# Kernel optimization log

Hardware: AMD Instinct MI355X
Metric: run time of the kernel (lower is better)

## Reference

```python
import jax, jax.numpy as jnp
import numpy as np

B, C, H = 256, 5, 13
N_AGENTS = 8192
N_EDGES = 262144
ACT = 21


def setup_inputs() -> dict:
    key = jax.random.key(0)
    ks = jax.random.split(key, 20)
    inp = {
        "x": jax.random.normal(ks[0], (B, C, H, H), jnp.float32),
        "x_msg": jax.random.normal(ks[1], (N_AGENTS,), jnp.float32),
        "edge_index": jax.random.randint(ks[2], (N_EDGES, 2), 0, N_AGENTS, jnp.int64 if jax.config.jax_enable_x64 else jnp.int32),
        "action": jax.random.randint(ks[3], (B,), 0, ACT, jnp.int32),
        # params (orthogonal init approximated by scaled normal; math identical)
        "conv1_w": jax.random.normal(ks[4], (32, 5, 3, 3), jnp.float32) * 0.1,
        "conv1_b": jnp.zeros((32,), jnp.float32),
        "conv2_w": jax.random.normal(ks[5], (64, 32, 3, 3), jnp.float32) * 0.05,
        "conv2_b": jnp.zeros((64,), jnp.float32),
        "fc_w": jax.random.normal(ks[6], (512, 1024), jnp.float32) * 0.03,
        "fc_b": jnp.zeros((512,), jnp.float32),
        "fc_mu_w": jax.random.normal(ks[7], (ACT, 512), jnp.float32) * 0.01,
        "fc_mu_b": jnp.zeros((ACT,), jnp.float32),
        "msg_w": jax.random.normal(ks[8], (N_AGENTS, 512), jnp.float32) * 0.01,
        "msg_b": jnp.zeros((N_AGENTS,), jnp.float32),
        "gcn1_w": jax.random.normal(ks[9], (2, 16), jnp.float32) * 0.5,
        "gcn1_b": jnp.zeros((16,), jnp.float32),
        "gcn2_w": jax.random.normal(ks[10], (16, N_AGENTS), jnp.float32) * 0.1,
        "gcn2_b": jnp.zeros((N_AGENTS,), jnp.float32),
    }
    return inp


def _gcn_norm(edge_index, n):
    # add self-loops; edge_index is (E,2) [src, dst]
    loops = jnp.arange(n, dtype=edge_index.dtype)
    src = jnp.concatenate([edge_index[:, 0], loops])
    dst = jnp.concatenate([edge_index[:, 1], loops])
    deg = jax.ops.segment_sum(jnp.ones_like(src, jnp.float32), dst, num_segments=n)
    dinv = jnp.where(deg > 0, jax.lax.rsqrt(deg), 0.0)
    norm = dinv[src] * dinv[dst]  # [E+n]
    return src, dst, norm


def _gcn_conv(h, src, dst, norm, W, b, n):
    hw = h @ W  # [n, out]
    out = jax.ops.segment_sum(norm[:, None] * hw[src], dst, num_segments=n)
    return out + b


def reference(x, x_msg, edge_index, action, conv1_w, conv1_b, conv2_w, conv2_b,
              fc_w, fc_b, fc_mu_w, fc_mu_b, msg_w, msg_b,
              gcn1_w, gcn1_b, gcn2_w, gcn2_b):
    dn = ("NCHW", "OIHW", "NCHW")
    h = jax.lax.conv_general_dilated(x, conv1_w, (2, 2), "VALID", dimension_numbers=dn)
    h = jax.nn.relu(h + conv1_b[None, :, None, None])  # [B,32,6,6]
    h = jax.lax.conv_general_dilated(h, conv2_w, (1, 1), "VALID", dimension_numbers=dn)
    h = jax.nn.relu(h + conv2_b[None, :, None, None])  # [B,64,4,4]
    h = h.reshape(h.shape[0], -1)  # [B,1024], torch NCHW flatten order
    hidden = jax.nn.relu(h @ fc_w.T + fc_b)  # [B,512]

    logits = hidden @ fc_mu_w.T + fc_mu_b            # [B,21]
    actor_encoding = hidden @ msg_w.T + msg_b        # [B,N]

    # Categorical log_prob / entropy for the given action
    logp = jax.nn.log_softmax(logits, axis=-1)
    log_prob = jnp.take_along_axis(logp, action[:, None], axis=1)[:, 0]
    entropy = -jnp.sum(jnp.exp(logp) * logp, axis=-1)

    # GNN message branch (eval mode: dropout is identity)
    feats = jnp.stack([x_msg, actor_encoding[0]], axis=0).T  # [N,2]
    n = feats.shape[0]
    src, dst, norm = _gcn_norm(edge_index, n)
    g = jax.nn.relu(_gcn_conv(feats, src, dst, norm, gcn1_w, gcn1_b, n))  # [N,16]
    g = _gcn_conv(g, src, dst, norm, gcn2_w, gcn2_b, n)                    # [N,N]
    msg_out = jax.nn.log_softmax(g, axis=1).mean(axis=1)                   # [N]

    return (action, msg_out, log_prob, entropy)
```

## Files before the change

kernel.cpp:

```cpp
#include <hip/hip_runtime.h>
#include <hip/hip_bf16.h>

#define NB 256
#define NACT 21
#define NA 8192
#define NE 262144
#define CSR_CAP 128
#define LOG2E 1.44269504f

#if __has_builtin(__builtin_amdgcn_exp2f)
#define EXP2F(x) __builtin_amdgcn_exp2f(x)
#else
#define EXP2F(x) exp2f(x)
#endif

typedef __attribute__((ext_vector_type(8))) short short8;
typedef __attribute__((ext_vector_type(4))) float float4v;

__device__ inline float wsum64(float v) {
#pragma unroll
  for (int m = 32; m > 0; m >>= 1) v += __shfl_xor(v, m, 64);
  return v;
}

__device__ inline unsigned short f2bf(float f) {
  union { __hip_bfloat16 h; unsigned short u; } cv;
  cv.h = __float2bfloat16(f);
  return cv.u;
}

__global__ __launch_bounds__(512, 2) void k_ip(
    const float* __restrict__ x, const float* __restrict__ c1w, const float* __restrict__ c1b_,
    const float* __restrict__ c2w, const float* __restrict__ fcw,
    const float* __restrict__ g2w, const float* __restrict__ g2b,
    unsigned short* c1b, unsigned short* w2abf, int* cnt,
    unsigned short* fcwbf, unsigned short* w2t, float* wpart) {
  __shared__ float sm[3437];
  int t = threadIdx.x, b = blockIdx.x;
  if (b >= 308) {
    float (*red)[17] = (float(*)[17])sm;
    float* b2s = sm + 272;
    int blk = b - 308;
    {
      int base = (blk * 512 + t) * 2;
      float2 v = *(const float2*)&fcw[base];
      fcwbf[base + 0] = f2bf(v.x);
      fcwbf[base + 1] = f2bf(v.y);
    }
    {
      if (t < 256) {
        int jj = t >> 4, k = t & 15;
        int j = blk * 16 + jj;
        float w = g2w[k * 8192 + j];
        w2t[j * 16 + k] = f2bf(w);
        red[jj][k] = w;
      }
      if (t < 16) b2s[t] = g2b[blk * 16 + t];
      __syncthreads();
      if (t < 16) {
        float s = 0.0f;
#pragma unroll
        for (int q = 0; q < 16; q++) s += red[q][t];
        wpart[blk * 17 + t] = s;
      } else if (t == 16) {
        float s = 0.0f;
#pragma unroll
        for (int q = 0; q < 16; q++) s += b2s[q];
        wpart[blk * 17 + 16] = s;
      }
    }
    return;
  }
  if (b >= 272) {
    int i = (b - 272) * 512 + t;
    w2abf[i] = f2bf(c2w[i]);
    return;
  }
  if (b >= 256) {
    cnt[(b - 256) * 512 + t] = 0;
    return;
  }
  float* xs = sm;
  float* w1s = sm + 845;
  float* c1s = sm + 2285;
  for (int i = t; i < 845; i += 512) xs[i] = x[b * 845 + i];
  for (int i = t; i < 1440; i += 512) w1s[i] = c1w[i];
  __syncthreads();
  for (int idx = t; idx < 1152; idx += 512) {
    int oc = idx / 36, p = idx - oc * 36;
    int oy = p / 6, ox = p - oy * 6;
    float acc = c1b_[oc];
    const float* wp = &w1s[oc * 45];
#pragma unroll
    for (int ic = 0; ic < 5; ic++)
#pragma unroll
      for (int ky = 0; ky < 3; ky++)
#pragma unroll
        for (int kx = 0; kx < 3; kx++)
          acc += xs[ic * 169 + (oy * 2 + ky) * 13 + ox * 2 + kx] * wp[ic * 9 + ky * 3 + kx];
    c1s[idx] = fmaxf(acc, 0.0f);
  }
  __syncthreads();
  for (int i = t; i < 4608; i += 512) {
    int p = i / 288, k = i - p * 288;
    int ic = k / 9, r = k - ic * 9;
    int ky = r / 3, kx = r - ky * 3;
    int oy = p >> 2, ox = p & 3;
    c1b[b * 4608 + i] = f2bf(c1s[ic * 36 + (oy + ky) * 6 + ox + kx]);
  }
}

__global__ __launch_bounds__(512, 2) void k_cf(
    const int* __restrict__ edges, int* cnt, int* csr,
    const unsigned short* __restrict__ c1b, const unsigned short* __restrict__ w2abf,
    const float* __restrict__ c2b, const unsigned short* __restrict__ fcwbf,
    const float* __restrict__ fcb, const float* __restrict__ wpart,
    float* hidden, float* wsf) {
  __shared__ __align__(16) unsigned short hs[16384];
  __shared__ __align__(16) unsigned short w2a[18432];
  __shared__ float red[2048];
  int t = threadIdx.x, blk = blockIdx.x;
  int wave = t >> 6, lane = t & 63;
  int m = lane & 15, quad = lane >> 4;
  if (blk >= 1024) {
    if (t < 272) {
      int q = t / 17, c = t - q * 17;
      float s = 0.0f;
      for (int r = q; r < 512; r += 16) s += wpart[r * 17 + c];
      red[t] = s;
    }
    __syncthreads();
    if (t < 17) {
      float s = 0.0f;
#pragma unroll
      for (int q = 0; q < 16; q++) s += red[q * 17 + t];
      wsf[t] = s;
    }
    return;
  }
  if (blk >= 512) {
    int e = (blk - 512) * 512 + t;
    int s = edges[2 * e], d = edges[2 * e + 1];
    int slot = atomicAdd(&cnt[d], 1);
    if (slot < CSR_CAP) csr[d * CSR_CAP + slot] = s;
    return;
  }
  for (int i = t; i < 2304; i += 512)
    *(short8*)&w2a[i * 8] = *(const short8*)&w2abf[i * 8];
  __syncthreads();
  int tr = blk >> 5, tc = blk & 31;
  {
    int nlb = wave * 32;
    int nbase = tr * 256 + nlb;
    float4v z = {0.0f, 0.0f, 0.0f, 0.0f};
    float4v acc00 = z, acc01 = z, acc02 = z, acc03 = z;
    float4v acc10 = z, acc11 = z, acc12 = z, acc13 = z;
#pragma unroll
    for (int ks = 0; ks < 9; ks++) {
      int ko = ks * 32 + quad * 8;
      short8 a0 = *(const short8*)&w2a[(0 * 16 + m) * 288 + ko];
      short8 a1 = *(const short8*)&w2a[(1 * 16 + m) * 288 + ko];
      short8 a2 = *(const short8*)&w2a[(2 * 16 + m) * 288 + ko];
      short8 a3 = *(const short8*)&w2a[(3 * 16 + m) * 288 + ko];
      short8 b0 = *(const short8*)&c1b[(nbase + m) * 288 + ko];
      short8 b1 = *(const short8*)&c1b[(nbase + 16 + m) * 288 + ko];
      acc00 = __builtin_amdgcn_mfma_f32_16x16x32_bf16(a0, b0, acc00, 0, 0, 0);
      acc01 = __builtin_amdgcn_mfma_f32_16x16x32_bf16(a1, b0, acc01, 0, 0, 0);
      acc02 = __builtin_amdgcn_mfma_f32_16x16x32_bf16(a2, b0, acc02, 0, 0, 0);
      acc03 = __builtin_amdgcn_mfma_f32_16x16x32_bf16(a3, b0, acc03, 0, 0, 0);
      acc10 = __builtin_amdgcn_mfma_f32_16x16x32_bf16(a0, b1, acc10, 0, 0, 0);
      acc11 = __builtin_amdgcn_mfma_f32_16x16x32_bf16(a1, b1, acc11, 0, 0, 0);
      acc12 = __builtin_amdgcn_mfma_f32_16x16x32_bf16(a2, b1, acc12, 0, 0, 0);
      acc13 = __builtin_amdgcn_mfma_f32_16x16x32_bf16(a3, b1, acc13, 0, 0, 0);
    }
    float4v accs[2][4] = {{acc00, acc01, acc02, acc03}, {acc10, acc11, acc12, acc13}};
#pragma unroll
    for (int nt = 0; nt < 2; nt++) {
#pragma unroll
      for (int mt = 0; mt < 4; mt++) {
#pragma unroll
        for (int r = 0; r < 4; r++) {
          int oc = mt * 16 + quad * 4 + r;
          int nl = nlb + nt * 16 + m;
          hs[(nl >> 4) * 1024 + oc * 16 + (nl & 15)] =
              f2bf(fmaxf(accs[nt][mt][r] + c2b[oc], 0.0f));
        }
      }
    }
  }
  __syncthreads();
  {
    const unsigned short* ap = &hs[m * 1024 + wave * 128 + quad * 8];
    const unsigned short* bp = &fcwbf[(tc * 16 + m) * 1024 + wave * 128 + quad * 8];
    float4v acc = {0.0f, 0.0f, 0.0f, 0.0f};
#pragma unroll
    for (int ks = 0; ks < 4; ks++) {
      short8 av = *(const short8*)(ap + ks * 32);
      short8 bv = *(const short8*)(bp + ks * 32);
      acc = __builtin_amdgcn_mfma_f32_16x16x32_bf16(av, bv, acc, 0, 0, 0);
    }
#pragma unroll
    for (int r = 0; r < 4; r++) red[wave * 256 + (quad * 4 + r) * 16 + m] = acc[r];
    __syncthreads();
    if (t < 256) {
      float s = 0.0f;
#pragma unroll
      for (int w = 0; w < 8; w++) s += red[w * 256 + t];
      int gr = tr * 16 + (t >> 4);
      int gc = tc * 16 + (t & 15);
      hidden[gr * 512 + gc] = fmaxf(s + fcb[gc], 0.0f);
    }
  }
}

__global__ __launch_bounds__(512, 2) void k_he(
    const float* __restrict__ hidden, const float* __restrict__ muw,
    const float* __restrict__ mub, const float* __restrict__ msgw,
    const float* __restrict__ msgb, const int* __restrict__ cnt,
    const float* __restrict__ x_msg, const int* __restrict__ action,
    float2* xe, float* dinv, float* out) {
  __shared__ float muT[10752];
  __shared__ float hrows[2048];
  int t = threadIdx.x, blk = blockIdx.x;
  int wave = t >> 6, lane = t & 63;
  if (blk >= 512) {
    int i = (blk - 512) * 512 + t;
    float d = rsqrtf((float)cnt[i] + 1.0f);
    dinv[i] = d;
    xe[i].x = d * x_msg[i];
    return;
  }
  if (blk < 64) {
    int b0 = blk * 4;
    for (int i = t; i < 10752; i += 512) {
      int a = i >> 9, k = i & 511;
      muT[k * 21 + a] = muw[i];
    }
    for (int i = t; i < 2048; i += 512) hrows[i] = hidden[b0 * 512 + i];
    __syncthreads();
    if (wave < 4) {
      int b = b0 + wave;
      float logit = -1e30f;
      if (lane < NACT) {
        float acc = mub[lane];
        const float* hr = &hrows[wave * 512];
        for (int k = 0; k < 512; k++) acc += hr[k] * muT[k * 21 + lane];
        logit = acc;
      }
      float mx = logit;
#pragma unroll
      for (int s = 32; s > 0; s >>= 1) mx = fmaxf(mx, __shfl_xor(mx, s, 64));
      float e = (lane < NACT) ? __expf(logit - mx) : 0.0f;
      float se = wsum64(e);
      float swl = wsum64(e * logit);
      float lse = mx + __logf(se);
      int act = action[b];
      if (lane == 0) {
        out[b] = (float)act;
        out[8704 + b] = lse - swl / se;
      }
      if (lane == act) out[8448 + b] = logit - lse;
    }
  } else {
    int wg = (blk - 64) * 8 + wave;
    for (int j = wg; j < NA; j += 3584) {
      const float* wp = &msgw[j * 512 + lane * 8];
      float4 w0 = *(const float4*)(wp);
      float4 w1 = *(const float4*)(wp + 4);
      float4 h0 = *(const float4*)&hidden[lane * 8];
      float4 h1 = *(const float4*)&hidden[lane * 8 + 4];
      float s = w0.x * h0.x + w0.y * h0.y + w0.z * h0.z + w0.w * h0.w +
                w1.x * h1.x + w1.y * h1.y + w1.z * h1.z + w1.w * h1.w;
      s = wsum64(s);
      if (lane == 0) xe[j].y = rsqrtf((float)cnt[j] + 1.0f) * (s + msgb[j]);
    }
  }
}

__global__ __launch_bounds__(512, 4) void k_g1(
    const int* __restrict__ cnt, const int* __restrict__ csr,
    const float* __restrict__ dinv, const float2* __restrict__ xe,
    const float* __restrict__ g1w, const float* __restrict__ g1b, float* gbuf2) {
  int t = threadIdx.x, blk = blockIdx.x;
  int wave = t >> 6, lane = t & 63;
  int wg = blk * 8 + wave;
#pragma unroll
  for (int rr = 0; rr < 2; rr++) {
    int i = wg * 2 + rr;
    int ci = min(cnt[i], CSR_CAP);
    float di = dinv[i];
    float a0 = 0.0f, a1 = 0.0f;
    for (int e = lane; e < ci; e += 64) {
      int s = csr[i * CSR_CAP + e];
      float2 v = xe[s];
      a0 += v.x;
      a1 += v.y;
    }
    float2 vi = xe[i];
    float f0 = (wsum64(a0) + vi.x) * di;
    float f1 = (wsum64(a1) + vi.y) * di;
    if (lane < 16) {
      float gv = fmaxf(f0 * g1w[lane] + f1 * g1w[16 + lane] + g1b[lane], 0.0f);
      gbuf2[i * 16 + lane] = di * gv;
    }
  }
}

__global__ __launch_bounds__(512, 4) void k_msg(
    const int* __restrict__ cnt, const int* __restrict__ csr,
    const float* __restrict__ dinv, const float* __restrict__ gbuf2,
    const float* __restrict__ wsf, const unsigned short* __restrict__ w2t,
    const float* __restrict__ g2b, float* out) {
  __shared__ __align__(16) unsigned short vbf[256];
  __shared__ float vf[256];
  __shared__ float pl[2048];
  __shared__ float sl[128];
  __shared__ float wsfs[17];
  int t = threadIdx.x, blk = blockIdx.x;
  int wave = t >> 6, lane = t & 63;
  int rowbase = blk * 16;
  if (t < 17) wsfs[t] = wsf[t];
  {
    int eq = lane >> 4, c = lane & 15;
#pragma unroll
    for (int rr = 0; rr < 2; rr++) {
      int il = wave * 2 + rr;
      int i = rowbase + il;
      int ci = min(cnt[i], CSR_CAP);
      float di = dinv[i];
      float acc = (eq == 0) ? gbuf2[i * 16 + c] : 0.0f;
      for (int e = eq; e < ci; e += 4) {
        int s = csr[i * CSR_CAP + e];
        acc += gbuf2[s * 16 + c];
      }
      acc *= di;
      acc += __shfl_xor(acc, 16, 64);
      acc += __shfl_xor(acc, 32, 64);
      if (eq == 0) {
        vf[il * 16 + c] = acc;
        vbf[il * 16 + c] = f2bf(acc * LOG2E);
      }
    }
  }
  __syncthreads();
  float myMean = 0.0f;
  if (t < 16) {
    float dot = 0.0f;
#pragma unroll
    for (int c = 0; c < 16; c++) dot += vf[t * 16 + c] * wsfs[c];
    myMean = (dot + wsfs[16]) * (1.0f / 8192.0f);
  }
  {
    int quad = lane >> 4, n = lane & 15;
    int k8 = quad * 8;
    short8 za = {0, 0, 0, 0, 0, 0, 0, 0};
    short8 a1 = za;
    if (quad < 2) a1 = *(const short8*)&vbf[n * 16 + k8];
    float sacc[4];
#pragma unroll
    for (int q = 0; q < 4; q++) sacc[q] = 0.0f;
    int colb = wave * 1024 + n;
    for (int tp = 0; tp < 64; tp += 2) {
      int col1 = colb + tp * 16;
      int col2 = col1 + 16;
      short8 b1 = za, b2 = za;
      if (quad < 2) {
        b1 = *(const short8*)&w2t[col1 * 16 + k8];
        b2 = *(const short8*)&w2t[col2 * 16 + k8];
      }
      float bb1 = g2b[col1] * LOG2E, bb2 = g2b[col2] * LOG2E;
      float4v c1 = {bb1, bb1, bb1, bb1};
      float4v c2 = {bb2, bb2, bb2, bb2};
      float4v s11 = __builtin_amdgcn_mfma_f32_16x16x32_bf16(a1, b1, c1, 0, 0, 0);
      float4v s12 = __builtin_amdgcn_mfma_f32_16x16x32_bf16(a1, b2, c2, 0, 0, 0);
#pragma unroll
      for (int r = 0; r < 4; r++) sacc[r] += EXP2F(s11[r]) + EXP2F(s12[r]);
    }
#pragma unroll
    for (int q = 0; q < 4; q++) {
      int rl = quad * 4 + q;
      pl[rl * 128 + wave * 16 + n] = sacc[q];
    }
  }
  __syncthreads();
  if (t < 128) {
    int r = t >> 3, seg = t & 7;
    int base = r * 128 + seg * 16;
    float ll = 0.0f;
#pragma unroll
    for (int i = 0; i < 16; i++) ll += pl[base + i];
    sl[r * 8 + seg] = ll;
  }
  __syncthreads();
  if (t < 16) {
    float ll = 0.0f;
#pragma unroll
    for (int i = 0; i < 8; i++) ll += sl[t * 8 + i];
    out[256 + rowbase + t] = myMean - __logf(ll);
  }
}

extern "C" void kernel_launch(void* const* d_in, const int* in_sizes, int n_in,
                              void* d_out, int out_size, void* d_ws, size_t ws_size,
                              hipStream_t stream) {
  const float* x     = (const float*)d_in[0];
  const float* x_msg = (const float*)d_in[1];
  const int*   edges = (const int*)d_in[2];
  const int*   action= (const int*)d_in[3];
  const float* c1w   = (const float*)d_in[4];
  const float* c1bb  = (const float*)d_in[5];
  const float* c2w   = (const float*)d_in[6];
  const float* c2b   = (const float*)d_in[7];
  const float* fcw   = (const float*)d_in[8];
  const float* fcb   = (const float*)d_in[9];
  const float* muw   = (const float*)d_in[10];
  const float* mub   = (const float*)d_in[11];
  const float* msgw  = (const float*)d_in[12];
  const float* msgb  = (const float*)d_in[13];
  const float* g1w   = (const float*)d_in[14];
  const float* g1b   = (const float*)d_in[15];
  const float* g2w   = (const float*)d_in[16];
  const float* g2b   = (const float*)d_in[17];
  float* out = (float*)d_out;

  float* ws     = (float*)d_ws;
  unsigned short* fcwbf   = (unsigned short*)(ws + 131072);
  float* hidden = ws + 393216;
  float2* xe    = (float2*)(ws + 524288);
  float* dinv   = ws + 540672;
  float* gbuf2  = ws + 548864;
  float* wpart  = ws + 679936;
  unsigned short* w2t = (unsigned short*)(ws + 688640);
  int*   cnt    = (int*)(ws + 754176);
  int*   csr    = (int*)(ws + 762368);
  float* wsf    = ws + 1810944;
  unsigned short* c1b   = (unsigned short*)(ws + 1810964);
  unsigned short* w2abf = (unsigned short*)(ws + 2400788);

  k_ip <<<820, 512, 0, stream>>>(x, c1w, c1bb, c2w, fcw, g2w, g2b,
                                 c1b, w2abf, cnt, fcwbf, w2t, wpart);
  k_cf <<<1025, 512, 0, stream>>>(edges, cnt, csr, c1b, w2abf, c2b,
                                  fcwbf, fcb, wpart, hidden, wsf);
  k_he <<<528, 512, 0, stream>>>(hidden, muw, mub, msgw, msgb, cnt, x_msg,
                                 action, xe, dinv, out);
  k_g1 <<<512, 512, 0, stream>>>(cnt, csr, dinv, xe, g1w, g1b, gbuf2);
  k_msg<<<512, 512, 0, stream>>>(cnt, csr, dinv, gbuf2, wsf, w2t, g2b, out);
}
```

Baseline: 170.4 us.

## Fuse conv2 into per-sample conv1 kernel and drop redundant conv2 recompute

Moves the conv2 MFMA from k_cf into k_ip, where each sample block now computes conv2 directly from its shared-memory im2col tile, converting the fp32 conv2 weights to bf16 on the fly. Only the 1024-wide bf16 activations go to global memory, instead of the larger im2col buffer and a separate bf16 weight buffer. Before, every k_cf block (32 per row-tile) recomputed the same conv2 tile; now k_cf only runs the fc GEMM and uses less shared memory (launch bounds raised to 4). In exchange, k_ip blocks do more work, with only 4 of 8 waves active for conv2, and every block re-reads and re-converts the conv2 weights from global memory.

After: 165.2 us. 1.03x faster.

```diff
diff --git a/kernel.cpp b/kernel.cpp
--- a/kernel.cpp
+++ b/kernel.cpp
@@ -31,16 +31,17 @@
 
 __global__ __launch_bounds__(512, 2) void k_ip(
     const float* __restrict__ x, const float* __restrict__ c1w, const float* __restrict__ c1b_,
-    const float* __restrict__ c2w, const float* __restrict__ fcw,
+    const float* __restrict__ c2w, const float* __restrict__ c2b, const float* __restrict__ fcw,
     const float* __restrict__ g2w, const float* __restrict__ g2b,
-    unsigned short* c1b, unsigned short* w2abf, int* cnt,
+    unsigned short* h1024bf, int* cnt,
     unsigned short* fcwbf, unsigned short* w2t, float* wpart) {
-  __shared__ float sm[3437];
+  __shared__ __align__(16) float sm[5744];
   int t = threadIdx.x, b = blockIdx.x;
-  if (b >= 308) {
+  int wave = t >> 6, lane = t & 63;
+  if (b >= 272) {
     float (*red)[17] = (float(*)[17])sm;
     float* b2s = sm + 272;
-    int blk = b - 308;
+    int blk = b - 272;
     {
       int base = (blk * 512 + t) * 2;
       float2 v = *(const float2*)&fcw[base];
@@ -71,11 +72,6 @@
     }
     return;
   }
-  if (b >= 272) {
-    int i = (b - 272) * 512 + t;
-    w2abf[i] = f2bf(c2w[i]);
-    return;
-  }
   if (b >= 256) {
     cnt[(b - 256) * 512 + t] = 0;
     return;
@@ -83,6 +79,7 @@
   float* xs = sm;
   float* w1s = sm + 845;
   float* c1s = sm + 2285;
+  unsigned short* c1bf = (unsigned short*)(sm + 3440);
   for (int i = t; i < 845; i += 512) xs[i] = x[b * 845 + i];
   for (int i = t; i < 1440; i += 512) w1s[i] = c1w[i];
   __syncthreads();
@@ -103,21 +100,42 @@
   __syncthreads();
   for (int i = t; i < 4608; i += 512) {
     int p = i / 288, k = i - p * 288;
-    int ic = k / 9, r = k - ic * 9;
-    int ky = r / 3, kx = r - ky * 3;
+    int ic = k / 9, rr = k - ic * 9;
+    int ky = rr / 3, kx = rr - ky * 3;
     int oy = p >> 2, ox = p & 3;
-    c1b[b * 4608 + i] = f2bf(c1s[ic * 36 + (oy + ky) * 6 + ox + kx]);
-  }
-}
-
-__global__ __launch_bounds__(512, 2) void k_cf(
+    c1bf[i] = f2bf(c1s[ic * 36 + (oy + ky) * 6 + ox + kx]);
+  }
+  __syncthreads();
+  if (wave < 4) {
+    int m = lane & 15, quad = lane >> 4;
+    float4v acc = {0.0f, 0.0f, 0.0f, 0.0f};
+#pragma unroll
+    for (int ks = 0; ks < 9; ks++) {
+      int ko = ks * 32 + quad * 8;
+      const float* ar = &c2w[(wave * 16 + m) * 288 + ko];
+      float4 af0 = *(const float4*)ar;
+      float4 af1 = *(const float4*)(ar + 4);
+      short8 a;
+      a[0] = (short)f2bf(af0.x); a[1] = (short)f2bf(af0.y);
+      a[2] = (short)f2bf(af0.z); a[3] = (short)f2bf(af0.w);
+      a[4] = (short)f2bf(af1.x); a[5] = (short)f2bf(af1.y);
+      a[6] = (short)f2bf(af1.z); a[7] = (short)f2bf(af1.w);
+      short8 bv = *(const short8*)&c1bf[m * 288 + ko];
+      acc = __builtin_amdgcn_mfma_f32_16x16x32_bf16(a, bv, acc, 0, 0, 0);
+    }
+#pragma unroll
+    for (int r = 0; r < 4; r++) {
+      int oc = wave * 16 + quad * 4 + r;
+      h1024bf[b * 1024 + oc * 16 + m] = f2bf(fmaxf(acc[r] + c2b[oc], 0.0f));
+    }
+  }
+}
+
+__global__ __launch_bounds__(512, 4) void k_cf(
     const int* __restrict__ edges, int* cnt, int* csr,
-    const unsigned short* __restrict__ c1b, const unsigned short* __restrict__ w2abf,
-    const float* __restrict__ c2b, const unsigned short* __restrict__ fcwbf,
+    const unsigned short* __restrict__ h1024bf, const unsigned short* __restrict__ fcwbf,
     const float* __restrict__ fcb, const float* __restrict__ wpart,
     float* hidden, float* wsf) {
-  __shared__ __align__(16) unsigned short hs[16384];
-  __shared__ __align__(16) unsigned short w2a[18432];
   __shared__ float red[2048];
   int t = threadIdx.x, blk = blockIdx.x;
   int wave = t >> 6, lane = t & 63;
@@ -145,71 +163,26 @@
     if (slot < CSR_CAP) csr[d * CSR_CAP + slot] = s;
     return;
   }
-  for (int i = t; i < 2304; i += 512)
-    *(short8*)&w2a[i * 8] = *(const short8*)&w2abf[i * 8];
-  __syncthreads();
   int tr = blk >> 5, tc = blk & 31;
-  {
-    int nlb = wave * 32;
-    int nbase = tr * 256 + nlb;
-    float4v z = {0.0f, 0.0f, 0.0f, 0.0f};
-    float4v acc00 = z, acc01 = z, acc02 = z, acc03 = z;
-    float4v acc10 = z, acc11 = z, acc12 = z, acc13 = z;
-#pragma unroll
-    for (int ks = 0; ks < 9; ks++) {
-      int ko = ks * 32 + quad * 8;
-      short8 a0 = *(const short8*)&w2a[(0 * 16 + m) * 288 + ko];
-      short8 a1 = *(const short8*)&w2a[(1 * 16 + m) * 288 + ko];
-      short8 a2 = *(const short8*)&w2a[(2 * 16 + m) * 288 + ko];
-      short8 a3 = *(const short8*)&w2a[(3 * 16 + m) * 288 + ko];
-      short8 b0 = *(const short8*)&c1b[(nbase + m) * 288 + ko];
-      short8 b1 = *(const short8*)&c1b[(nbase + 16 + m) * 288 + ko];
-      acc00 = __builtin_amdgcn_mfma_f32_16x16x32_bf16(a0, b0, acc00, 0, 0, 0);
-      acc01 = __builtin_amdgcn_mfma_f32_16x16x32_bf16(a1, b0, acc01, 0, 0, 0);
-      acc02 = __builtin_amdgcn_mfma_f32_16x16x32_bf16(a2, b0, acc02, 0, 0, 0);
-      acc03 = __builtin_amdgcn_mfma_f32_16x16x32_bf16(a3, b0, acc03, 0, 0, 0);
-      acc10 = __builtin_amdgcn_mfma_f32_16x16x32_bf16(a0, b1, acc10, 0, 0, 0);
-      acc11 = __builtin_amdgcn_mfma_f32_16x16x32_bf16(a1, b1, acc11, 0, 0, 0);
-      acc12 = __builtin_amdgcn_mfma_f32_16x16x32_bf16(a2, b1, acc12, 0, 0, 0);
-      acc13 = __builtin_amdgcn_mfma_f32_16x16x32_bf16(a3, b1, acc13, 0, 0, 0);
-    }
-    float4v accs[2][4] = {{acc00, acc01, acc02, acc03}, {acc10, acc11, acc12, acc13}};
-#pragma unroll
-    for (int nt = 0; nt < 2; nt++) {
-#pragma unroll
-      for (int mt = 0; mt < 4; mt++) {
-#pragma unroll
-        for (int r = 0; r < 4; r++) {
-          int oc = mt * 16 + quad * 4 + r;
-          int nl = nlb + nt * 16 + m;
-          hs[(nl >> 4) * 1024 + oc * 16 + (nl & 15)] =
-              f2bf(fmaxf(accs[nt][mt][r] + c2b[oc], 0.0f));
-        }
-      }
-    }
-  }
-  __syncthreads();
-  {
-    const unsigned short* ap = &hs[m * 1024 + wave * 128 + quad * 8];
-    const unsigned short* bp = &fcwbf[(tc * 16 + m) * 1024 + wave * 128 + quad * 8];
-    float4v acc = {0.0f, 0.0f, 0.0f, 0.0f};
-#pragma unroll
-    for (int ks = 0; ks < 4; ks++) {
-      short8 av = *(const short8*)(ap + ks * 32);
-      short8 bv = *(const short8*)(bp + ks * 32);
-      acc = __builtin_amdgcn_mfma_f32_16x16x32_bf16(av, bv, acc, 0, 0, 0);
-    }
-#pragma unroll
-    for (int r = 0; r < 4; r++) red[wave * 256 + (quad * 4 + r) * 16 + m] = acc[r];
-    __syncthreads();
-    if (t < 256) {
-      float s = 0.0f;
-#pragma unroll
-      for (int w = 0; w < 8; w++) s += red[w * 256 + t];
-      int gr = tr * 16 + (t >> 4);
-      int gc = tc * 16 + (t & 15);
-      hidden[gr * 512 + gc] = fmaxf(s + fcb[gc], 0.0f);
-    }
+  const unsigned short* ap = &h1024bf[(tr * 16 + m) * 1024 + wave * 128 + quad * 8];
+  const unsigned short* bp = &fcwbf[(tc * 16 + m) * 1024 + wave * 128 + quad * 8];
+  float4v acc = {0.0f, 0.0f, 0.0f, 0.0f};
+#pragma unroll
+  for (int ks = 0; ks < 4; ks++) {
+    short8 av = *(const short8*)(ap + ks * 32);
+    short8 bv = *(const short8*)(bp + ks * 32);
+    acc = __builtin_amdgcn_mfma_f32_16x16x32_bf16(av, bv, acc, 0, 0, 0);
+  }
+#pragma unroll
+  for (int r = 0; r < 4; r++) red[wave * 256 + (quad * 4 + r) * 16 + m] = acc[r];
+  __syncthreads();
+  if (t < 256) {
+    float s = 0.0f;
+#pragma unroll
+    for (int w = 0; w < 8; w++) s += red[w * 256 + t];
+    int gr = tr * 16 + (t >> 4);
+    int gc = tc * 16 + (t & 15);
+    hidden[gr * 512 + gc] = fmaxf(s + fcb[gc], 0.0f);
   }
 }
 
@@ -424,6 +397,7 @@
   float* out = (float*)d_out;
 
   float* ws     = (float*)d_ws;
+  unsigned short* h1024bf = (unsigned short*)ws;
   unsigned short* fcwbf   = (unsigned short*)(ws + 131072);
   float* hidden = ws + 393216;
   float2* xe    = (float2*)(ws + 524288);
@@ -434,13 +408,11 @@
   int*   cnt    = (int*)(ws + 754176);
   int*   csr    = (int*)(ws + 762368);
   float* wsf    = ws + 1810944;
-  unsigned short* c1b   = (unsigned short*)(ws + 1810964);
-  unsigned short* w2abf = (unsigned short*)(ws + 2400788);
-
-  k_ip <<<820, 512, 0, stream>>>(x, c1w, c1bb, c2w, fcw, g2w, g2b,
-                                 c1b, w2abf, cnt, fcwbf, w2t, wpart);
-  k_cf <<<1025, 512, 0, stream>>>(edges, cnt, csr, c1b, w2abf, c2b,
-                                  fcwbf, fcb, wpart, hidden, wsf);
+
+  k_ip <<<784, 512, 0, stream>>>(x, c1w, c1bb, c2w, c2b, fcw, g2w, g2b,
+                                 h1024bf, cnt, fcwbf, w2t, wpart);
+  k_cf <<<1025, 512, 0, stream>>>(edges, cnt, csr, h1024bf, fcwbf, fcb, wpart,
+                                  hidden, wsf);
   k_he <<<528, 512, 0, stream>>>(hidden, muw, mub, msgw, msgb, cnt, x_msg,
                                  action, xe, dinv, out);
   k_g1 <<<512, 512, 0, stream>>>(cnt, csr, dinv, xe, g1w, g1b, gbuf2);
```
